# Kernel optimization log

Hardware: AMD Instinct MI355X
Metric: run time of the kernel (lower is better)

## Reference

```python
import jax, jax.numpy as jnp
import numpy as np

B, T, DIM, NH = 4, 2048, 1024, 16
HD = DIM // NH


def setup_inputs() -> dict:
    key = jax.random.key(0)
    ks = jax.random.split(key, 9)
    s = 0.02
    return {
        "x": jax.random.normal(ks[0], (B, T, DIM), dtype=jnp.float32),
        "Wq": jax.random.normal(ks[1], (DIM, DIM), dtype=jnp.float32) * s,
        "bq": jnp.zeros((DIM,), dtype=jnp.float32),
        "Wk": jax.random.normal(ks[2], (DIM, DIM), dtype=jnp.float32) * s,
        "bk": jnp.zeros((DIM,), dtype=jnp.float32),
        "Wv": jax.random.normal(ks[3], (DIM, DIM), dtype=jnp.float32) * s,
        "bv": jnp.zeros((DIM,), dtype=jnp.float32),
        "Wo": jax.random.normal(ks[4], (DIM, DIM), dtype=jnp.float32) * s,
        "bo": jnp.zeros((DIM,), dtype=jnp.float32),
    }


def reference(x, Wq, bq, Wk, bk, Wv, bv, Wo, bo):
    scale = HD ** -0.5
    # QKV projections (torch Linear: x @ W.T + b; here W stored as [in, out])
    q = (x @ Wq + bq).reshape(B, T, NH, HD).transpose(0, 2, 1, 3)  # [B,H,T,D]
    k = (x @ Wk + bk).reshape(B, T, NH, HD).transpose(0, 2, 1, 3)
    v = (x @ Wv + bv).reshape(B, T, NH, HD).transpose(0, 2, 1, 3)
    scores = jnp.einsum("bhqd,bhkd->bhqk", q, k) * scale  # [B,H,T,T]
    attn = jax.nn.softmax(scores, axis=-1)
    out = jnp.einsum("bhqk,bhkd->bhqd", attn, v)  # [B,H,T,D]
    out = out.transpose(0, 2, 1, 3).reshape(B, T, DIM)
    return out @ Wo + bo
```

## Files before the change

kernel.cpp:

```cpp
#include <hip/hip_runtime.h>
#include <math.h>

#define BB   4
#define TT   2048
#define DIMM 1024
#define NHH  16
#define HDD  64
#define MM   (BB * TT)

typedef unsigned short u16;
typedef unsigned int   u32;
typedef short bf16x8 __attribute__((ext_vector_type(8)));
typedef float f32x4  __attribute__((ext_vector_type(4)));

__device__ __forceinline__ u16 f2bf(float f) {
    u32 u = __float_as_uint(f);
    return (u16)((u + 0x7fffu + ((u >> 16) & 1u)) >> 16);
}

__device__ __forceinline__ f32x4 mfma16(bf16x8 a, bf16x8 b, f32x4 c) {
    return __builtin_amdgcn_mfma_f32_16x16x32_bf16(a, b, c, 0, 0, 0);
}

__device__ __forceinline__ int swz8(int row, int slot) {
    return ((slot ^ (row & 7) ^ ((row >> 3) & 7)) & 7) * 8;
}
__device__ __forceinline__ int swz4(int row, int slot) {
    return ((slot ^ (row & 3)) & 3) * 8;
}

__global__ void convert_x_bf16(const float* __restrict__ in, u16* __restrict__ out) {
    int i = (blockIdx.x * 256 + threadIdx.x) * 8;
    float4 a = *(const float4*)(in + i);
    float4 b = *(const float4*)(in + i + 4);
    u32 w0 = f2bf(a.x) | ((u32)f2bf(a.y) << 16);
    u32 w1 = f2bf(a.z) | ((u32)f2bf(a.w) << 16);
    u32 w2 = f2bf(b.x) | ((u32)f2bf(b.y) << 16);
    u32 w3 = f2bf(b.z) | ((u32)f2bf(b.w) << 16);
    uint4 o = make_uint4(w0, w1, w2, w3);
    *(uint4*)(out + i) = o;
}

__global__ void transpose_w_bf16(const float* __restrict__ W, u16* __restrict__ Wt) {
    __shared__ float tile[32][33];
    const int c  = threadIdx.x & 31;
    const int r8 = threadIdx.x >> 5;
    const int kb = blockIdx.y * 32, nb = blockIdx.x * 32;
#pragma unroll
    for (int rr = 0; rr < 4; ++rr) {
        int r = r8 + rr * 8;
        tile[r][c] = W[(kb + r) * 1024 + nb + c];
    }
    __syncthreads();
#pragma unroll
    for (int rr = 0; rr < 4; ++rr) {
        int r = r8 + rr * 8;
        Wt[(nb + r) * 1024 + kb + c] = f2bf(tile[c][r]);
    }
}

__global__ __launch_bounds__(256, 2) void gemm_qkv(
    const u16* __restrict__ A, const u16* __restrict__ Bt,
    const float* __restrict__ bq, const float* __restrict__ bk,
    const float* __restrict__ bv,
    u16* __restrict__ Qout, u16* __restrict__ Kout, u16* __restrict__ Vout,
    float qscale)
{
    __shared__ u16 As[128 * 32];
    __shared__ u16 Bs[128 * 32];

    const int tid  = threadIdx.x;
    const int m0   = blockIdx.x * 128;
    const int n0   = blockIdx.y * 128;
    const int wave = tid >> 6, lane = tid & 63;
    const int wr = wave >> 1, wc = wave & 1;
    const int l15 = lane & 15, l4 = lane >> 4;

    const int r0 = tid >> 2, ks = tid & 3;
    const int r1 = r0 + 64;
    const int w0 = r0 * 32 + swz4(r0, ks);
    const int w1 = r1 * 32 + swz4(r1, ks);

    f32x4 acc[4][4];
#pragma unroll
    for (int i = 0; i < 4; ++i)
#pragma unroll
        for (int j = 0; j < 4; ++j) acc[i][j] = (f32x4){0.f, 0.f, 0.f, 0.f};

    const u16* Ar0 = A  + (m0 + r0) * 1024 + ks * 8;
    const u16* Ar1 = A  + (m0 + r1) * 1024 + ks * 8;
    const u16* Br0 = Bt + (n0 + r0) * 1024 + ks * 8;
    const u16* Br1 = Bt + (n0 + r1) * 1024 + ks * 8;

    uint4 a0 = *(const uint4*)Ar0;
    uint4 a1 = *(const uint4*)Ar1;
    uint4 b0 = *(const uint4*)Br0;
    uint4 b1 = *(const uint4*)Br1;
    *(uint4*)&As[w0] = a0; *(uint4*)&As[w1] = a1;
    *(uint4*)&Bs[w0] = b0; *(uint4*)&Bs[w1] = b1;
    __syncthreads();

    for (int kt = 0; kt < 32; ++kt) {
        if (kt < 31) {
            const int ko = (kt + 1) * 32;
            a0 = *(const uint4*)(Ar0 + ko);
            a1 = *(const uint4*)(Ar1 + ko);
            b0 = *(const uint4*)(Br0 + ko);
            b1 = *(const uint4*)(Br1 + ko);
        }
        bf16x8 af[4], bf[4];
#pragma unroll
        for (int rt = 0; rt < 4; ++rt) {
            int row = wr * 64 + rt * 16 + l15;
            af[rt] = *(const bf16x8*)&As[row * 32 + swz4(row, l4)];
            int col = wc * 64 + rt * 16 + l15;
            bf[rt] = *(const bf16x8*)&Bs[col * 32 + swz4(col, l4)];
        }
#pragma unroll
        for (int rt = 0; rt < 4; ++rt)
#pragma unroll
            for (int ct = 0; ct < 4; ++ct)
                acc[rt][ct] = mfma16(af[rt], bf[ct], acc[rt][ct]);
        __syncthreads();
        if (kt < 31) {
            *(uint4*)&As[w0] = a0; *(uint4*)&As[w1] = a1;
            *(uint4*)&Bs[w0] = b0; *(uint4*)&Bs[w1] = b1;
            __syncthreads();
        }
    }

    const int mode = n0 >> 10;
    const float* bias = (mode == 0) ? bq : (mode == 1) ? bk : bv;
    const float osc = (mode == 0) ? qscale : 1.0f;
    u16* Sout = (mode == 0) ? Qout : Kout;

#pragma unroll
    for (int rt = 0; rt < 4; ++rt)
#pragma unroll
        for (int ct = 0; ct < 4; ++ct) {
            int n  = n0 + wc * 64 + ct * 16 + l15;
            int nn = n & 1023;
            float bn = bias[nn];
            int h = nn >> 6, d = nn & 63;
            if (mode == 2) {
                int m00 = m0 + wr * 64 + rt * 16 + l4 * 4;
                int b = m00 >> 11, t0 = m00 & 2047;
                ushort4 pk;
                pk.x = f2bf(acc[rt][ct][0] + bn);
                pk.y = f2bf(acc[rt][ct][1] + bn);
                pk.z = f2bf(acc[rt][ct][2] + bn);
                pk.w = f2bf(acc[rt][ct][3] + bn);
                *(ushort4*)(&Vout[((((b << 4) + h) * 64 + d) << 11) + t0]) = pk;
            } else {
#pragma unroll
                for (int i = 0; i < 4; ++i) {
                    int m = m0 + wr * 64 + rt * 16 + l4 * 4 + i;
                    int b = m >> 11, t = m & 2047;
                    Sout[(((b << 4) + h) * 2048 + t) * 64 + d] =
                        f2bf((acc[rt][ct][i] + bn) * osc);
                }
            }
        }
}

__global__ __launch_bounds__(256, 2) void gemm_out(
    const u16* __restrict__ A, const u16* __restrict__ Bt,
    const float* __restrict__ bias, float* __restrict__ Cout)
{
    __shared__ u16 As[128 * 32];
    __shared__ u16 Bs[128 * 32];

    const int tid  = threadIdx.x;
    const int m0   = blockIdx.x * 128;
    const int n0   = blockIdx.y * 128;
    const int wave = tid >> 6, lane = tid & 63;
    const int wr = wave >> 1, wc = wave & 1;
    const int l15 = lane & 15, l4 = lane >> 4;

    const int r0 = tid >> 2, ks = tid & 3;
    const int r1 = r0 + 64;
    const int w0 = r0 * 32 + swz4(r0, ks);
    const int w1 = r1 * 32 + swz4(r1, ks);

    f32x4 acc[4][4];
#pragma unroll
    for (int i = 0; i < 4; ++i)
#pragma unroll
        for (int j = 0; j < 4; ++j) acc[i][j] = (f32x4){0.f, 0.f, 0.f, 0.f};

    const u16* Ar0 = A  + (m0 + r0) * 1024 + ks * 8;
    const u16* Ar1 = A  + (m0 + r1) * 1024 + ks * 8;
    const u16* Br0 = Bt + (n0 + r0) * 1024 + ks * 8;
    const u16* Br1 = Bt + (n0 + r1) * 1024 + ks * 8;

    uint4 a0 = *(const uint4*)Ar0;
    uint4 a1 = *(const uint4*)Ar1;
    uint4 b0 = *(const uint4*)Br0;
    uint4 b1 = *(const uint4*)Br1;
    *(uint4*)&As[w0] = a0; *(uint4*)&As[w1] = a1;
    *(uint4*)&Bs[w0] = b0; *(uint4*)&Bs[w1] = b1;
    __syncthreads();

    for (int kt = 0; kt < 32; ++kt) {
        if (kt < 31) {
            const int ko = (kt + 1) * 32;
            a0 = *(const uint4*)(Ar0 + ko);
            a1 = *(const uint4*)(Ar1 + ko);
            b0 = *(const uint4*)(Br0 + ko);
            b1 = *(const uint4*)(Br1 + ko);
        }
        bf16x8 af[4], bf[4];
#pragma unroll
        for (int rt = 0; rt < 4; ++rt) {
            int row = wr * 64 + rt * 16 + l15;
            af[rt] = *(const bf16x8*)&As[row * 32 + swz4(row, l4)];
            int col = wc * 64 + rt * 16 + l15;
            bf[rt] = *(const bf16x8*)&Bs[col * 32 + swz4(col, l4)];
        }
#pragma unroll
        for (int rt = 0; rt < 4; ++rt)
#pragma unroll
            for (int ct = 0; ct < 4; ++ct)
                acc[rt][ct] = mfma16(af[rt], bf[ct], acc[rt][ct]);
        __syncthreads();
        if (kt < 31) {
            *(uint4*)&As[w0] = a0; *(uint4*)&As[w1] = a1;
            *(uint4*)&Bs[w0] = b0; *(uint4*)&Bs[w1] = b1;
            __syncthreads();
        }
    }

#pragma unroll
    for (int rt = 0; rt < 4; ++rt)
#pragma unroll
        for (int ct = 0; ct < 4; ++ct) {
            int n = n0 + wc * 64 + ct * 16 + l15;
            float bn = bias[n];
#pragma unroll
            for (int i = 0; i < 4; ++i) {
                int m = m0 + wr * 64 + rt * 16 + l4 * 4 + i;
                Cout[m * 1024 + n] = acc[rt][ct][i] + bn;
            }
        }
}

__global__ __launch_bounds__(256, 4) void attn_mfma(
    const u16* __restrict__ Qb, const u16* __restrict__ Kb,
    const u16* __restrict__ Vtg, u16* __restrict__ Ob)
{
    __shared__ u16 Ks[2][64 * 64];
    __shared__ u16 Vts[2][64 * 64];
    __shared__ u16 Ps[4][16 * 64];

    const int tid   = threadIdx.x;
    const int g     = blockIdx.x;
    const int chunk = (g & 7) * 256 + (g >> 3);
    const int bh    = chunk >> 5;
    const int q0    = (chunk & 31) * 64;
    const int b     = bh >> 4, h = bh & 15;
    const u16* Qp   = Qb + (bh * TT + q0) * HDD;
    const u16* Kp   = Kb + bh * TT * HDD;
    const u16* Vp   = Vtg + bh * TT * HDD;

    const int wave = tid >> 6, lane = tid & 63;
    const int l15 = lane & 15, l4 = lane >> 4;

    bf16x8 qf[2];
#pragma unroll
    for (int hf = 0; hf < 2; ++hf)
        qf[hf] = *(const bf16x8*)(Qp + (wave * 16 + l15) * HDD + hf * 32 + l4 * 8);

    f32x4 oacc[4];
    float mr = -INFINITY, lr = 0.f;
#pragma unroll
    for (int db = 0; db < 4; ++db) oacc[db] = (f32x4){0.f, 0.f, 0.f, 0.f};

    const int pxor = (l15 & 7) ^ ((l15 >> 3) << 2);
    u32* const Pw = (u32*)&Ps[wave][0];
    int pidx[8];
#pragma unroll
    for (int nt = 0; nt < 4; ++nt)
#pragma unroll
        for (int pp = 0; pp < 2; ++pp) {
            int k2 = nt * 16 + l4 * 4 + 2 * pp;
            int slotW = ((k2 >> 3) ^ pxor) & 7;
            pidx[nt * 2 + pp] = (l15 * 64 + slotW * 8 + (k2 & 7)) >> 1;
        }
    int pread[2];
#pragma unroll
    for (int hf = 0; hf < 2; ++hf)
        pread[hf] = l15 * 64 + ((((hf << 2) + l4) ^ pxor) & 7) * 8;

    const int r0 = tid >> 3, ds = tid & 7;
    const int r1 = r0 + 32;
    const int wo0 = r0 * 64 + swz8(r0, ds);
    const int wo1 = r1 * 64 + swz8(r1, ds);

    uint4 kr0, kr1, vr0, vr1;
    kr0 = *(const uint4*)(Kp + r0 * 64 + ds * 8);
    kr1 = *(const uint4*)(Kp + r1 * 64 + ds * 8);
    vr0 = *(const uint4*)(Vp + r0 * 2048 + ds * 8);
    vr1 = *(const uint4*)(Vp + r1 * 2048 + ds * 8);
    *(uint4*)&Ks[0][wo0]  = kr0;
    *(uint4*)&Ks[0][wo1]  = kr1;
    *(uint4*)&Vts[0][wo0] = vr0;
    *(uint4*)&Vts[0][wo1] = vr1;
    __syncthreads();

    for (int kv = 0; kv < TT / 64; ++kv) {
        const int cur = kv & 1;

        if (kv < TT / 64 - 1) {
            const u16* Kt = Kp + (kv + 1) * 64 * HDD;
            const u16* Vt = Vp + (kv + 1) * 64;
            kr0 = *(const uint4*)(Kt + r0 * 64 + ds * 8);
            kr1 = *(const uint4*)(Kt + r1 * 64 + ds * 8);
            vr0 = *(const uint4*)(Vt + r0 * 2048 + ds * 8);
            vr1 = *(const uint4*)(Vt + r1 * 2048 + ds * 8);
        }

        f32x4 sacc[4];
#pragma unroll
        for (int nt = 0; nt < 4; ++nt) sacc[nt] = (f32x4){0.f, 0.f, 0.f, 0.f};
        __builtin_amdgcn_s_setprio(1);
#pragma unroll
        for (int nt = 0; nt < 4; ++nt) {
            int krow = nt * 16 + l15;
#pragma unroll
            for (int hf = 0; hf < 2; ++hf) {
                bf16x8 kf = *(const bf16x8*)&Ks[cur][krow * 64 + swz8(krow, hf * 4 + l4)];
                sacc[nt] = mfma16(kf, qf[hf], sacc[nt]);
            }
        }
        __builtin_amdgcn_s_setprio(0);

        auto pack_pass = [&]() -> float {
            float ls = 0.f;
#pragma unroll
            for (int nt = 0; nt < 4; ++nt)
#pragma unroll
                for (int pp = 0; pp < 2; ++pp) {
                    float pa = exp2f(sacc[nt][2 * pp]     - mr);
                    float pb = exp2f(sacc[nt][2 * pp + 1] - mr);
                    ls += pa + pb;
                    u32 pk;
                    asm("v_cvt_pk_bf16_f32 %0, %1, %2" : "=v"(pk) : "v"(pa), "v"(pb));
                    Pw[pidx[nt * 2 + pp]] = pk;
                }
            return ls;
        };
        float lsum = pack_pass();
        float ls2 = lsum + __shfl_xor(lsum, 16, 64);
        ls2 += __shfl_xor(ls2, 32, 64);
        if (__builtin_expect(__any(!(ls2 < 1e30f)), 0)) {
            float mx = sacc[0][0];
#pragma unroll
            for (int nt = 0; nt < 4; ++nt)
#pragma unroll
                for (int i = 0; i < 4; ++i) mx = fmaxf(mx, sacc[nt][i]);
            mx = fmaxf(mx, __shfl_xor(mx, 16, 64));
            mx = fmaxf(mx, __shfl_xor(mx, 32, 64));
            float mnew = fmaxf(mr, mx);
            float rsc  = exp2f(mr - mnew);
            mr = mnew;
            lr *= rsc;
            float rr[4];
#pragma unroll
            for (int i = 0; i < 4; ++i) rr[i] = __shfl(rsc, l4 * 4 + i, 16);
#pragma unroll
            for (int db = 0; db < 4; ++db)
#pragma unroll
                for (int i = 0; i < 4; ++i) oacc[db][i] *= rr[i];
            lsum = pack_pass();
            ls2 = lsum + __shfl_xor(lsum, 16, 64);
            ls2 += __shfl_xor(ls2, 32, 64);
        }
        lr += ls2;

        bf16x8 pf[2];
#pragma unroll
        for (int hf = 0; hf < 2; ++hf)
            pf[hf] = *(const bf16x8*)&Ps[wave][pread[hf]];
        __builtin_amdgcn_s_setprio(1);
#pragma unroll
        for (int db = 0; db < 4; ++db) {
            int d = db * 16 + l15;
#pragma unroll
            for (int hf = 0; hf < 2; ++hf) {
                bf16x8 vf = *(const bf16x8*)&Vts[cur][d * 64 + swz8(d, hf * 4 + l4)];
                oacc[db] = mfma16(pf[hf], vf, oacc[db]);
            }
        }
        __builtin_amdgcn_s_setprio(0);

        if (kv < TT / 64 - 1) {
            const int nxt = cur ^ 1;
            *(uint4*)&Ks[nxt][wo0]  = kr0;
            *(uint4*)&Ks[nxt][wo1]  = kr1;
            *(uint4*)&Vts[nxt][wo0] = vr0;
            *(uint4*)&Vts[nxt][wo1] = vr1;
        }
        __syncthreads();
    }

    float inv[4];
#pragma unroll
    for (int i = 0; i < 4; ++i) inv[i] = 1.f / __shfl(lr, l4 * 4 + i, 16);
#pragma unroll
    for (int db = 0; db < 4; ++db)
#pragma unroll
        for (int i = 0; i < 4; ++i) {
            int t   = q0 + wave * 16 + l4 * 4 + i;
            int col = h * 64 + db * 16 + l15;
            Ob[(b * TT + t) * DIMM + col] = f2bf(oacc[db][i] * inv[i]);
        }
}

extern "C" void kernel_launch(void* const* d_in, const int* in_sizes, int n_in,
                              void* d_out, int out_size, void* d_ws, size_t ws_size,
                              hipStream_t stream)
{
    const float* x  = (const float*)d_in[0];
    const float* Wq = (const float*)d_in[1];
    const float* bq = (const float*)d_in[2];
    const float* Wk = (const float*)d_in[3];
    const float* bk = (const float*)d_in[4];
    const float* Wv = (const float*)d_in[5];
    const float* bv = (const float*)d_in[6];
    const float* Wo = (const float*)d_in[7];
    const float* bo = (const float*)d_in[8];

    u16* xb   = (u16*)d_ws;
    u16* wcat = xb   + 8388608;
    u16* wot  = wcat + 3145728;
    u16* qbuf = wot  + 1048576;
    u16* obuf = qbuf + 8388608;
    u16* kbuf = (u16*)d_out;
    u16* vbuf = kbuf + 8388608;

    convert_x_bf16<<<4096, 256, 0, stream>>>(x, xb);
    transpose_w_bf16<<<dim3(32, 32), 256, 0, stream>>>(Wq, wcat);
    transpose_w_bf16<<<dim3(32, 32), 256, 0, stream>>>(Wk, wcat + 1048576);
    transpose_w_bf16<<<dim3(32, 32), 256, 0, stream>>>(Wv, wcat + 2097152);
    transpose_w_bf16<<<dim3(32, 32), 256, 0, stream>>>(Wo, wot);

    const float qscale = 0.125f * 1.44269504f;
    gemm_qkv<<<dim3(MM / 128, 3 * DIMM / 128), 256, 0, stream>>>(
        xb, wcat, bq, bk, bv, qbuf, kbuf, vbuf, qscale);

    attn_mfma<<<BB * NHH * (TT / 64), 256, 0, stream>>>(qbuf, kbuf, vbuf, obuf);

    gemm_out<<<dim3(MM / 128, DIMM / 128), 256, 0, stream>>>(obuf, wot, bo,
                                                             (float*)d_out);
}
```

Before: 242.6 us.

## Use direct global-to-LDS loads with double-buffered LDS in GEMMs and attention

Replaces the register-staged global loads and LDS stores in both GEMMs and the attention kernel with global_load_lds direct transfers. The GEMMs also move to double-buffered LDS, which drops one barrier per k-step. Swizzling is now applied on the global-address side, so the LDS layout stays compatible with the existing fragment reads. This aims to cut VGPR pressure and the LDS-store instructions, at the cost of doubled GEMM LDS use and reliance on the barrier waiting for outstanding LDS-DMA loads.

```diff
diff --git a/kernel.cpp b/kernel.cpp
--- a/kernel.cpp
+++ b/kernel.cpp
@@ -20,6 +20,12 @@
 
 __device__ __forceinline__ f32x4 mfma16(bf16x8 a, bf16x8 b, f32x4 c) {
     return __builtin_amdgcn_mfma_f32_16x16x32_bf16(a, b, c, 0, 0, 0);
+}
+
+__device__ __forceinline__ void gl_lds16(const u16* g, u16* l) {
+    __builtin_amdgcn_global_load_lds(
+        (const __attribute__((address_space(1))) void*)g,
+        (__attribute__((address_space(3))) void*)l, 16, 0, 0);
 }
 
 __device__ __forceinline__ int swz8(int row, int slot) {
@@ -59,6 +65,7 @@
     }
 }
 
+
 __global__ __launch_bounds__(256, 2) void gemm_qkv(
     const u16* __restrict__ A, const u16* __restrict__ Bt,
     const float* __restrict__ bq, const float* __restrict__ bk,
@@ -66,8 +73,8 @@
     u16* __restrict__ Qout, u16* __restrict__ Kout, u16* __restrict__ Vout,
     float qscale)
 {
-    __shared__ u16 As[128 * 32];
-    __shared__ u16 Bs[128 * 32];
+    __shared__ u16 As[2][128 * 32];
+    __shared__ u16 Bs[2][128 * 32];
 
     const int tid  = threadIdx.x;
     const int m0   = blockIdx.x * 128;
@@ -76,10 +83,17 @@
     const int wr = wave >> 1, wc = wave & 1;
     const int l15 = lane & 15, l4 = lane >> 4;
 
-    const int r0 = tid >> 2, ks = tid & 3;
-    const int r1 = r0 + 64;
-    const int w0 = r0 * 32 + swz4(r0, ks);
-    const int w1 = r1 * 32 + swz4(r1, ks);
+    int aOff[2], sOff[2];
+#pragma unroll
+    for (int c = 0; c < 2; ++c) {
+        int rbase = 32 * wave + 16 * c;
+        int row   = rbase + (lane >> 2);
+        int slot  = (lane & 3) ^ (row & 3);
+        aOff[c] = row * 1024 + slot * 8;
+        sOff[c] = rbase * 32;
+    }
+    const u16* Ab = A  + m0 * 1024;
+    const u16* Bb = Bt + n0 * 1024;
 
     f32x4 acc[4][4];
 #pragma unroll
@@ -87,34 +101,30 @@
 #pragma unroll
         for (int j = 0; j < 4; ++j) acc[i][j] = (f32x4){0.f, 0.f, 0.f, 0.f};
 
-    const u16* Ar0 = A  + (m0 + r0) * 1024 + ks * 8;
-    const u16* Ar1 = A  + (m0 + r1) * 1024 + ks * 8;
-    const u16* Br0 = Bt + (n0 + r0) * 1024 + ks * 8;
-    const u16* Br1 = Bt + (n0 + r1) * 1024 + ks * 8;
-
-    uint4 a0 = *(const uint4*)Ar0;
-    uint4 a1 = *(const uint4*)Ar1;
-    uint4 b0 = *(const uint4*)Br0;
-    uint4 b1 = *(const uint4*)Br1;
-    *(uint4*)&As[w0] = a0; *(uint4*)&As[w1] = a1;
-    *(uint4*)&Bs[w0] = b0; *(uint4*)&Bs[w1] = b1;
+#pragma unroll
+    for (int c = 0; c < 2; ++c) {
+        gl_lds16(Ab + aOff[c], &As[0][sOff[c]]);
+        gl_lds16(Bb + aOff[c], &Bs[0][sOff[c]]);
+    }
     __syncthreads();
 
+    int buf = 0;
     for (int kt = 0; kt < 32; ++kt) {
         if (kt < 31) {
             const int ko = (kt + 1) * 32;
-            a0 = *(const uint4*)(Ar0 + ko);
-            a1 = *(const uint4*)(Ar1 + ko);
-            b0 = *(const uint4*)(Br0 + ko);
-            b1 = *(const uint4*)(Br1 + ko);
+#pragma unroll
+            for (int c = 0; c < 2; ++c) {
+                gl_lds16(Ab + ko + aOff[c], &As[buf ^ 1][sOff[c]]);
+                gl_lds16(Bb + ko + aOff[c], &Bs[buf ^ 1][sOff[c]]);
+            }
         }
         bf16x8 af[4], bf[4];
 #pragma unroll
         for (int rt = 0; rt < 4; ++rt) {
             int row = wr * 64 + rt * 16 + l15;
-            af[rt] = *(const bf16x8*)&As[row * 32 + swz4(row, l4)];
+            af[rt] = *(const bf16x8*)&As[buf][row * 32 + swz4(row, l4)];
             int col = wc * 64 + rt * 16 + l15;
-            bf[rt] = *(const bf16x8*)&Bs[col * 32 + swz4(col, l4)];
+            bf[rt] = *(const bf16x8*)&Bs[buf][col * 32 + swz4(col, l4)];
         }
 #pragma unroll
         for (int rt = 0; rt < 4; ++rt)
@@ -122,11 +132,7 @@
             for (int ct = 0; ct < 4; ++ct)
                 acc[rt][ct] = mfma16(af[rt], bf[ct], acc[rt][ct]);
         __syncthreads();
-        if (kt < 31) {
-            *(uint4*)&As[w0] = a0; *(uint4*)&As[w1] = a1;
-            *(uint4*)&Bs[w0] = b0; *(uint4*)&Bs[w1] = b1;
-            __syncthreads();
-        }
+        buf ^= 1;
     }
 
     const int mode = n0 >> 10;
@@ -167,8 +173,8 @@
     const u16* __restrict__ A, const u16* __restrict__ Bt,
     const float* __restrict__ bias, float* __restrict__ Cout)
 {
-    __shared__ u16 As[128 * 32];
-    __shared__ u16 Bs[128 * 32];
+    __shared__ u16 As[2][128 * 32];
+    __shared__ u16 Bs[2][128 * 32];
 
     const int tid  = threadIdx.x;
     const int m0   = blockIdx.x * 128;
@@ -177,10 +183,17 @@
     const int wr = wave >> 1, wc = wave & 1;
     const int l15 = lane & 15, l4 = lane >> 4;
 
-    const int r0 = tid >> 2, ks = tid & 3;
-    const int r1 = r0 + 64;
-    const int w0 = r0 * 32 + swz4(r0, ks);
-    const int w1 = r1 * 32 + swz4(r1, ks);
+    int aOff[2], sOff[2];
+#pragma unroll
+    for (int c = 0; c < 2; ++c) {
+        int rbase = 32 * wave + 16 * c;
+        int row   = rbase + (lane >> 2);
+        int slot  = (lane & 3) ^ (row & 3);
+        aOff[c] = row * 1024 + slot * 8;
+        sOff[c] = rbase * 32;
+    }
+    const u16* Ab = A  + m0 * 1024;
+    const u16* Bb = Bt + n0 * 1024;
 
     f32x4 acc[4][4];
 #pragma unroll
@@ -188,34 +201,30 @@
 #pragma unroll
         for (int j = 0; j < 4; ++j) acc[i][j] = (f32x4){0.f, 0.f, 0.f, 0.f};
 
-    const u16* Ar0 = A  + (m0 + r0) * 1024 + ks * 8;
-    const u16* Ar1 = A  + (m0 + r1) * 1024 + ks * 8;
-    const u16* Br0 = Bt + (n0 + r0) * 1024 + ks * 8;
-    const u16* Br1 = Bt + (n0 + r1) * 1024 + ks * 8;
-
-    uint4 a0 = *(const uint4*)Ar0;
-    uint4 a1 = *(const uint4*)Ar1;
-    uint4 b0 = *(const uint4*)Br0;
-    uint4 b1 = *(const uint4*)Br1;
-    *(uint4*)&As[w0] = a0; *(uint4*)&As[w1] = a1;
-    *(uint4*)&Bs[w0] = b0; *(uint4*)&Bs[w1] = b1;
+#pragma unroll
+    for (int c = 0; c < 2; ++c) {
+        gl_lds16(Ab + aOff[c], &As[0][sOff[c]]);
+        gl_lds16(Bb + aOff[c], &Bs[0][sOff[c]]);
+    }
     __syncthreads();
 
+    int buf = 0;
     for (int kt = 0; kt < 32; ++kt) {
         if (kt < 31) {
             const int ko = (kt + 1) * 32;
-            a0 = *(const uint4*)(Ar0 + ko);
-            a1 = *(const uint4*)(Ar1 + ko);
-            b0 = *(const uint4*)(Br0 + ko);
-            b1 = *(const uint4*)(Br1 + ko);
+#pragma unroll
+            for (int c = 0; c < 2; ++c) {
+                gl_lds16(Ab + ko + aOff[c], &As[buf ^ 1][sOff[c]]);
+                gl_lds16(Bb + ko + aOff[c], &Bs[buf ^ 1][sOff[c]]);
+            }
         }
         bf16x8 af[4], bf[4];
 #pragma unroll
         for (int rt = 0; rt < 4; ++rt) {
             int row = wr * 64 + rt * 16 + l15;
-            af[rt] = *(const bf16x8*)&As[row * 32 + swz4(row, l4)];
+            af[rt] = *(const bf16x8*)&As[buf][row * 32 + swz4(row, l4)];
             int col = wc * 64 + rt * 16 + l15;
-            bf[rt] = *(const bf16x8*)&Bs[col * 32 + swz4(col, l4)];
+            bf[rt] = *(const bf16x8*)&Bs[buf][col * 32 + swz4(col, l4)];
         }
 #pragma unroll
         for (int rt = 0; rt < 4; ++rt)
@@ -223,11 +232,7 @@
             for (int ct = 0; ct < 4; ++ct)
                 acc[rt][ct] = mfma16(af[rt], bf[ct], acc[rt][ct]);
         __syncthreads();
-        if (kt < 31) {
-            *(uint4*)&As[w0] = a0; *(uint4*)&As[w1] = a1;
-            *(uint4*)&Bs[w0] = b0; *(uint4*)&Bs[w1] = b1;
-            __syncthreads();
-        }
+        buf ^= 1;
     }
 
 #pragma unroll
@@ -291,20 +296,22 @@
     for (int hf = 0; hf < 2; ++hf)
         pread[hf] = l15 * 64 + ((((hf << 2) + l4) ^ pxor) & 7) * 8;
 
-    const int r0 = tid >> 3, ds = tid & 7;
-    const int r1 = r0 + 32;
-    const int wo0 = r0 * 64 + swz8(r0, ds);
-    const int wo1 = r1 * 64 + swz8(r1, ds);
-
-    uint4 kr0, kr1, vr0, vr1;
-    kr0 = *(const uint4*)(Kp + r0 * 64 + ds * 8);
-    kr1 = *(const uint4*)(Kp + r1 * 64 + ds * 8);
-    vr0 = *(const uint4*)(Vp + r0 * 2048 + ds * 8);
-    vr1 = *(const uint4*)(Vp + r1 * 2048 + ds * 8);
-    *(uint4*)&Ks[0][wo0]  = kr0;
-    *(uint4*)&Ks[0][wo1]  = kr1;
-    *(uint4*)&Vts[0][wo0] = vr0;
-    *(uint4*)&Vts[0][wo1] = vr1;
+    int kOff[2], vOff[2], sBase[2];
+#pragma unroll
+    for (int c = 0; c < 2; ++c) {
+        int rbase = 8 * wave + 32 * c;
+        int row   = rbase + (lane >> 3);
+        int slot  = (lane & 7) ^ (row & 7) ^ ((row >> 3) & 7);
+        kOff[c]  = row * 64 + slot * 8;
+        vOff[c]  = row * 2048 + slot * 8;
+        sBase[c] = rbase * 64;
+    }
+
+#pragma unroll
+    for (int c = 0; c < 2; ++c) {
+        gl_lds16(Kp + kOff[c], &Ks[0][sBase[c]]);
+        gl_lds16(Vp + vOff[c], &Vts[0][sBase[c]]);
+    }
     __syncthreads();
 
     for (int kv = 0; kv < TT / 64; ++kv) {
@@ -313,10 +320,11 @@
         if (kv < TT / 64 - 1) {
             const u16* Kt = Kp + (kv + 1) * 64 * HDD;
             const u16* Vt = Vp + (kv + 1) * 64;
-            kr0 = *(const uint4*)(Kt + r0 * 64 + ds * 8);
-            kr1 = *(const uint4*)(Kt + r1 * 64 + ds * 8);
-            vr0 = *(const uint4*)(Vt + r0 * 2048 + ds * 8);
-            vr1 = *(const uint4*)(Vt + r1 * 2048 + ds * 8);
+#pragma unroll
+            for (int c = 0; c < 2; ++c) {
+                gl_lds16(Kt + kOff[c], &Ks[cur ^ 1][sBase[c]]);
+                gl_lds16(Vt + vOff[c], &Vts[cur ^ 1][sBase[c]]);
+            }
         }
 
         f32x4 sacc[4];
@@ -393,13 +401,6 @@
         }
         __builtin_amdgcn_s_setprio(0);
 
-        if (kv < TT / 64 - 1) {
-            const int nxt = cur ^ 1;
-            *(uint4*)&Ks[nxt][wo0]  = kr0;
-            *(uint4*)&Ks[nxt][wo1]  = kr1;
-            *(uint4*)&Vts[nxt][wo0] = vr0;
-            *(uint4*)&Vts[nxt][wo1] = vr1;
-        }
         __syncthreads();
     }
 
```

Result: slower. 253.9 us (+4.6%).
